# Kernel tuning notes

Hardware: AMD Instinct MI355X
Metric: run time of the kernel (lower is better)

Reference implementation:

```python
import jax, jax.numpy as jnp
import numpy as np

DIM = 512
HEADS = 16
HEAD_DIM = DIM // HEADS
WH, WW = 7, 7
N = WH * WW
OUP = 512
SCALE = HEAD_DIM ** -0.5
NW = 64  # windows per image (mask leading dim)


def _relative_position_index():
    coords = np.stack(np.meshgrid(np.arange(WH), np.arange(WW), indexing='ij'))  # (2,Wh,Ww)
    flat = coords.reshape(2, -1)                           # (2, N)
    rel = flat[:, :, None] - flat[:, None, :]              # (2, N, N)
    rel = rel.transpose(1, 2, 0).astype(np.int64)          # (N, N, 2)
    rel[:, :, 0] += WH - 1
    rel[:, :, 1] += WW - 1
    rel[:, :, 0] *= 2 * WW - 1
    return jnp.asarray(rel.sum(-1))                        # (N, N) int

REL_IDX = _relative_position_index()


def setup_inputs() -> dict:
    key = jax.random.key(0)
    ks = jax.random.split(key, 8)
    B_ = 4096
    x = jax.random.normal(ks[0], (B_, N, DIM), dtype=jnp.float32)
    mask = jnp.zeros((NW, N, N), dtype=jnp.float32)
    qkv_w = jax.random.normal(ks[1], (3 * DIM, DIM), dtype=jnp.float32) * (DIM ** -0.5)
    qkv_b = jax.random.normal(ks[2], (3 * DIM,), dtype=jnp.float32) * 0.02
    table = jax.random.normal(ks[3], ((2 * WH - 1) * (2 * WW - 1), HEADS), dtype=jnp.float32) * 0.02
    proj_w = jax.random.normal(ks[4], (OUP, DIM), dtype=jnp.float32) * (DIM ** -0.5)
    proj_b = jax.random.normal(ks[5], (OUP,), dtype=jnp.float32) * 0.02
    return {"x": x, "mask": mask, "qkv_w": qkv_w, "qkv_b": qkv_b,
            "table": table, "proj_w": proj_w, "proj_b": proj_b}


def reference(x, mask, qkv_w, qkv_b, table, proj_w, proj_b):
    B_, n, c = x.shape
    qkv = x @ qkv_w.T + qkv_b                               # (B_, N, 3C)
    qkv = qkv.reshape(B_, n, 3, HEADS, HEAD_DIM).transpose(2, 0, 3, 1, 4)
    q, k, v = qkv[0], qkv[1], qkv[2]                        # (B_, H, N, hd)
    q = q * SCALE
    attn = jnp.einsum('bhnd,bhmd->bhnm', q, k)              # (B_, H, N, N)
    bias = table[REL_IDX]                                   # (N, N, H) gather
    attn = attn + bias.transpose(2, 0, 1)[None]             # add rel-pos bias
    nW = mask.shape[0]
    attn = attn.reshape(B_ // nW, nW, HEADS, n, n) + mask[None, :, None]
    attn = attn.reshape(B_, HEADS, n, n)
    attn = jax.nn.softmax(attn, axis=-1)
    out = jnp.einsum('bhnm,bhmd->bhnd', attn, v)            # (B_, H, N, hd)
    out = out.transpose(0, 2, 1, 3).reshape(B_, n, c)
    return out @ proj_w.T + proj_b
```

## Files before the change

kernel.cpp:

```cpp
#include <hip/hip_runtime.h>
#include <hip/hip_bf16.h>
#include <stdint.h>

#define DIMC 512
#define HEADS 16
#define HEAD_DIM 32
#define NTOK 49
#define SCALE 0.17677669529663687f

typedef unsigned short u16;
typedef short bf16x8 __attribute__((ext_vector_type(8)));
typedef float f32x4 __attribute__((ext_vector_type(4)));
typedef u16 u16x4 __attribute__((ext_vector_type(4)));

#define MFMA16(a, b, c) __builtin_amdgcn_mfma_f32_16x16x32_bf16((a), (b), (c), 0, 0, 0)

__device__ __forceinline__ u16 f2bf(float f) {
  __hip_bfloat16 h = __float2bfloat16(f);
  u16 u;
  __builtin_memcpy(&u, &h, 2);
  return u;
}

__device__ __forceinline__ void gld16(const void* g, void* l) {
  __builtin_amdgcn_global_load_lds(
      (const __attribute__((address_space(1))) uint32_t*)g,
      (__attribute__((address_space(3))) uint32_t*)l, 16, 0, 0);
}

__global__ void cvt_f32_bf16(const float* __restrict__ in, u16* __restrict__ out, int n) {
  int i = (blockIdx.x * 256 + threadIdx.x) * 4;
  if (i < n) {
    float4 v = *(const float4*)(in + i);
    u16x4 r;
    r.x = f2bf(v.x); r.y = f2bf(v.y); r.z = f2bf(v.z); r.w = f2bf(v.w);
    *(u16x4*)(out + i) = r;
  }
}

__global__ void biasmask_kernel(const float* __restrict__ table, const float* __restrict__ mask,
                                float* __restrict__ bm) {
  const int wm = blockIdx.x >> 4;
  const int h  = blockIdx.x & 15;
  for (int e = threadIdx.x; e < 4096; e += 256) {
    const int i = e >> 6, j = e & 63;
    float v;
    if (i < NTOK && j < NTOK) {
      const int yi = i / 7, xi = i % 7, yj = j / 7, xj = j % 7;
      const int idx = (yi - yj + 6) * 13 + (xi - xj + 6);
      v = table[idx * HEADS + h] + mask[wm * (NTOK * NTOK) + i * NTOK + j];
    } else {
      v = -1e30f;
    }
    bm[(size_t)blockIdx.x * 4096 + e] = v;
  }
}

template<bool A_F32, bool OUT_BF16, bool QKV_SCALE>
__global__ void gemm_tn(const void* __restrict__ Ap, const u16* __restrict__ Bp,
                        const float* __restrict__ bias, void* __restrict__ Cp,
                        int M, int N, int K) {
  constexpr int ASTR = A_F32 ? 40 : 32;
  __shared__ u16 As[128 * ASTR];
  __shared__ u16 Bs[128 * 32];
  const int t = threadIdx.x;
  const int lane = t & 63;
  const int wv = t >> 6, wr = wv >> 1, wc = wv & 1;
  const int lr = lane & 15, lg = lane >> 4;
  const int bn0 = blockIdx.x * 128;
  const int bm0 = blockIdx.y * 128;

  f32x4 acc[4][4] = {};

  const int c0 = t, c1 = t + 256;
  const int nK = K >> 5;

  for (int kt = 0; kt < nK; ++kt) {
    const int k0 = kt << 5;
    __syncthreads();
    gld16(Bp + (size_t)(bn0 + (c0 >> 2)) * K + k0 + (c0 & 3) * 8, Bs + c0 * 8);
    gld16(Bp + (size_t)(bn0 + (c1 >> 2)) * K + k0 + (c1 & 3) * 8, Bs + c1 * 8);
    if (A_F32) {
      const float* A = (const float*)Ap;
      const float* src = A + (size_t)(bm0 + (t >> 1)) * K + k0 + (t & 1) * 16;
      float4 v0 = ((const float4*)src)[0];
      float4 v1 = ((const float4*)src)[1];
      float4 v2 = ((const float4*)src)[2];
      float4 v3 = ((const float4*)src)[3];
      bf16x8 p0, p1;
      p0[0] = f2bf(v0.x); p0[1] = f2bf(v0.y); p0[2] = f2bf(v0.z); p0[3] = f2bf(v0.w);
      p0[4] = f2bf(v1.x); p0[5] = f2bf(v1.y); p0[6] = f2bf(v1.z); p0[7] = f2bf(v1.w);
      p1[0] = f2bf(v2.x); p1[1] = f2bf(v2.y); p1[2] = f2bf(v2.z); p1[3] = f2bf(v2.w);
      p1[4] = f2bf(v3.x); p1[5] = f2bf(v3.y); p1[6] = f2bf(v3.z); p1[7] = f2bf(v3.w);
      u16* dst = &As[(t >> 1) * ASTR + (t & 1) * 16];
      *(bf16x8*)dst = p0;
      *(bf16x8*)(dst + 8) = p1;
    } else {
      const u16* A = (const u16*)Ap;
      gld16(A + (size_t)(bm0 + (c0 >> 2)) * K + k0 + (c0 & 3) * 8, As + c0 * 8);
      gld16(A + (size_t)(bm0 + (c1 >> 2)) * K + k0 + (c1 & 3) * 8, As + c1 * 8);
    }
    __syncthreads();

    bf16x8 af[4], bfr[4];
#pragma unroll
    for (int i = 0; i < 4; ++i)
      af[i] = *(const bf16x8*)&As[(wr * 64 + i * 16 + lr) * ASTR + lg * 8];
#pragma unroll
    for (int j = 0; j < 4; ++j)
      bfr[j] = *(const bf16x8*)&Bs[(wc * 64 + j * 16 + lr) * 32 + lg * 8];
#pragma unroll
    for (int i = 0; i < 4; ++i)
#pragma unroll
      for (int j = 0; j < 4; ++j)
        acc[i][j] = MFMA16(af[i], bfr[j], acc[i][j]);
  }

#pragma unroll
  for (int j = 0; j < 4; ++j) {
    const int col = bn0 + wc * 64 + j * 16 + lr;
    const float bv = bias[col];
    const float sc = (QKV_SCALE && col < DIMC) ? SCALE : 1.0f;
#pragma unroll
    for (int i = 0; i < 4; ++i) {
      const int row0 = bm0 + wr * 64 + i * 16 + lg * 4;
#pragma unroll
      for (int r = 0; r < 4; ++r) {
        const float val = (acc[i][j][r] + bv) * sc;
        if (OUT_BF16)
          ((u16*)Cp)[(size_t)(row0 + r) * N + col] = f2bf(val);
        else
          ((float*)Cp)[(size_t)(row0 + r) * N + col] = val;
      }
    }
  }
}

__global__ void attn_win(const u16* __restrict__ qkv, const float* __restrict__ bmask,
                         u16* __restrict__ aout) {
  __shared__ u16 P[4][64 * 72];
  const int t = threadIdx.x, lane = t & 63, wv = t >> 6;
  const int lr = lane & 15, lg = lane >> 4;
  const int w = blockIdx.x >> 2;
  const int h = ((blockIdx.x & 3) << 2) + wv;
  const size_t base = (size_t)w * NTOK * 1536 + h * HEAD_DIM;

  const bf16x8 zf = {};
  bf16x8 qf[4], kf[4];
#pragma unroll
  for (int i = 0; i < 4; ++i) {
    const int row = i * 16 + lr;
    const size_t roff = base + (size_t)row * 1536 + lg * 8;
    qf[i] = (row < NTOK) ? *(const bf16x8*)&qkv[roff] : zf;
    kf[i] = (row < NTOK) ? *(const bf16x8*)&qkv[roff + DIMC] : zf;
  }

  const f32x4 zc = {};
  f32x4 s[4][4];
#pragma unroll
  for (int i = 0; i < 4; ++i)
#pragma unroll
    for (int j = 0; j < 4; ++j)
      s[i][j] = MFMA16(qf[i], kf[j], zc);

  const float* bmp = bmask + (((size_t)(w & 63) * HEADS + h) << 12);
#pragma unroll
  for (int i = 0; i < 4; ++i)
#pragma unroll
    for (int r = 0; r < 4; ++r) {
      const int ii = i * 16 + lg * 4 + r;
#pragma unroll
      for (int j = 0; j < 4; ++j)
        s[i][j][r] += bmp[ii * 64 + j * 16 + lr];
    }

#pragma unroll
  for (int i = 0; i < 4; ++i)
#pragma unroll
    for (int r = 0; r < 4; ++r) {
      float m = fmaxf(fmaxf(s[i][0][r], s[i][1][r]), fmaxf(s[i][2][r], s[i][3][r]));
      m = fmaxf(m, __shfl_xor(m, 1));
      m = fmaxf(m, __shfl_xor(m, 2));
      m = fmaxf(m, __shfl_xor(m, 4));
      m = fmaxf(m, __shfl_xor(m, 8));
      float sum = 0.f;
#pragma unroll
      for (int j = 0; j < 4; ++j) {
        const float e = __expf(s[i][j][r] - m);
        s[i][j][r] = e;
        sum += e;
      }
      sum += __shfl_xor(sum, 1);
      sum += __shfl_xor(sum, 2);
      sum += __shfl_xor(sum, 4);
      sum += __shfl_xor(sum, 8);
      const float rinv = __builtin_amdgcn_rcpf(sum);
#pragma unroll
      for (int j = 0; j < 4; ++j) s[i][j][r] *= rinv;
    }

  u16* Pw = &P[wv][0];
#pragma unroll
  for (int i = 0; i < 4; ++i)
#pragma unroll
    for (int r = 0; r < 4; ++r) {
      const int ii = i * 16 + lg * 4 + r;
#pragma unroll
      for (int j = 0; j < 4; ++j)
        Pw[ii * 72 + j * 16 + lr] = f2bf(s[i][j][r]);
    }

  f32x4 o[4][2] = {};
#pragma unroll
  for (int ks = 0; ks < 2; ++ks) {
    bf16x8 vf[2];
#pragma unroll
    for (int dn = 0; dn < 2; ++dn) {
#pragma unroll
      for (int e = 0; e < 8; ++e) {
        int kk = ks * 32 + lg * 8 + e;
        kk = kk < NTOK ? kk : 0;
        vf[dn][e] = (short)qkv[base + 2 * DIMC + (size_t)kk * 1536 + dn * 16 + lr];
      }
    }
#pragma unroll
    for (int i = 0; i < 4; ++i) {
      const bf16x8 pa = *(const bf16x8*)&Pw[(i * 16 + lr) * 72 + ks * 32 + lg * 8];
#pragma unroll
      for (int dn = 0; dn < 2; ++dn)
        o[i][dn] = MFMA16(pa, vf[dn], o[i][dn]);
    }
  }

#pragma unroll
  for (int i = 0; i < 4; ++i)
#pragma unroll
    for (int r = 0; r < 4; ++r) {
      const int row = i * 16 + lg * 4 + r;
      if (row < NTOK) {
        const size_t ob = ((size_t)w * NTOK + row) * DIMC + h * HEAD_DIM;
#pragma unroll
        for (int dn = 0; dn < 2; ++dn)
          aout[ob + dn * 16 + lr] = f2bf(o[i][dn][r]);
      }
    }
}

extern "C" void kernel_launch(void* const* d_in, const int* in_sizes, int n_in,
                              void* d_out, int out_size, void* d_ws, size_t ws_size,
                              hipStream_t stream) {
  const float* x      = (const float*)d_in[0];
  const float* mask   = (const float*)d_in[1];
  const float* qkv_w  = (const float*)d_in[2];
  const float* qkv_b  = (const float*)d_in[3];
  const float* table  = (const float*)d_in[4];
  const float* proj_w = (const float*)d_in[5];
  const float* proj_b = (const float*)d_in[6];
  float* out = (float*)d_out;

  const int M = 4096 * NTOK;

  char* ws = (char*)d_ws;
  u16*   qkv_bf   = (u16*)ws;
  u16*   wqkv_bf  = (u16*)(ws + 616562688ull);
  u16*   wproj_bf = (u16*)(ws + 618135552ull);
  float* biasmask = (float*)(ws + 618659840ull);
  u16*   attn_bf  = (u16*)(ws + 635437056ull);

  cvt_f32_bf16<<<768, 256, 0, stream>>>(qkv_w, wqkv_bf, 1536 * 512);
  cvt_f32_bf16<<<256, 256, 0, stream>>>(proj_w, wproj_bf, 512 * 512);
  biasmask_kernel<<<1024, 256, 0, stream>>>(table, mask, biasmask);

  dim3 g1(1536 / 128, M / 128);
  gemm_tn<true, true, true><<<g1, 256, 0, stream>>>(x, wqkv_bf, qkv_b, qkv_bf, M, 1536, 512);

  attn_win<<<4096 * 4, 256, 0, stream>>>(qkv_bf, biasmask, attn_bf);

  dim3 g2(512 / 128, M / 128);
  gemm_tn<false, false, false><<<g2, 256, 0, stream>>>(attn_bf, wproj_bf, proj_b, out, M, 512, 512);
}
```

Before: 1.186 ms.

## Pre-convert x to bf16 and use swizzled K=64 GEMM tiles with block remapping

Adds a separate pass that converts x to bf16, so both GEMMs load their A operand through direct global-to-LDS loads instead of converting fp32 inside the tile loop. The GEMM now uses a 64-wide K tile with an XOR-swizzled LDS layout to avoid bank conflicts, and halves the number of barrier iterations. Blocks are launched on a 1D grid and remapped in strided groups of eight to improve L2 locality. The conversion kernel becomes a grid-stride loop handling eight elements per thread. The cost is an extra full read and write of x through the new conversion pass.

```diff
diff --git a/kernel.cpp b/kernel.cpp
--- a/kernel.cpp
+++ b/kernel.cpp
@@ -12,6 +12,7 @@
 typedef short bf16x8 __attribute__((ext_vector_type(8)));
 typedef float f32x4 __attribute__((ext_vector_type(4)));
 typedef u16 u16x4 __attribute__((ext_vector_type(4)));
+typedef u16 u16x8 __attribute__((ext_vector_type(8)));
 
 #define MFMA16(a, b, c) __builtin_amdgcn_mfma_f32_16x16x32_bf16((a), (b), (c), 0, 0, 0)
 
@@ -29,12 +30,14 @@
 }
 
 __global__ void cvt_f32_bf16(const float* __restrict__ in, u16* __restrict__ out, int n) {
-  int i = (blockIdx.x * 256 + threadIdx.x) * 4;
-  if (i < n) {
-    float4 v = *(const float4*)(in + i);
-    u16x4 r;
-    r.x = f2bf(v.x); r.y = f2bf(v.y); r.z = f2bf(v.z); r.w = f2bf(v.w);
-    *(u16x4*)(out + i) = r;
+  const int stride = gridDim.x * blockDim.x;
+  for (int i = blockIdx.x * blockDim.x + threadIdx.x; i * 8 < n; i += stride) {
+    const float4 v0 = ((const float4*)(in + i * 8))[0];
+    const float4 v1 = ((const float4*)(in + i * 8))[1];
+    u16x8 r;
+    r[0] = f2bf(v0.x); r[1] = f2bf(v0.y); r[2] = f2bf(v0.z); r[3] = f2bf(v0.w);
+    r[4] = f2bf(v1.x); r[5] = f2bf(v1.y); r[6] = f2bf(v1.z); r[7] = f2bf(v1.w);
+    *(u16x8*)(out + i * 8) = r;
   }
 }
 
@@ -56,64 +59,64 @@
   }
 }
 
-template<bool A_F32, bool OUT_BF16, bool QKV_SCALE>
-__global__ void gemm_tn(const void* __restrict__ Ap, const u16* __restrict__ Bp,
-                        const float* __restrict__ bias, void* __restrict__ Cp,
-                        int M, int N, int K) {
-  constexpr int ASTR = A_F32 ? 40 : 32;
-  __shared__ u16 As[128 * ASTR];
-  __shared__ u16 Bs[128 * 32];
+template<bool OUT_BF16, bool QKV_SCALE>
+__global__ void gemm_bf16(const u16* __restrict__ Ap, const u16* __restrict__ Bp,
+                          const float* __restrict__ bias, void* __restrict__ Cp,
+                          int M, int N, int K, int nxt) {
+  __shared__ u16 As[128 * 64];
+  __shared__ u16 Bs[128 * 64];
   const int t = threadIdx.x;
   const int lane = t & 63;
+  const int q = gridDim.x >> 3;
+  const int lin = blockIdx.x;
+  const int l = (lin & 7) * q + (lin >> 3);
+  const int bm0 = (l / nxt) * 128;
+  const int bn0 = (l % nxt) * 128;
   const int wv = t >> 6, wr = wv >> 1, wc = wv & 1;
   const int lr = lane & 15, lg = lane >> 4;
-  const int bn0 = blockIdx.x * 128;
-  const int bm0 = blockIdx.y * 128;
 
   f32x4 acc[4][4] = {};
 
-  const int c0 = t, c1 = t + 256;
-  const int nK = K >> 5;
-
+  int soff[4];
+#pragma unroll
+  for (int k = 0; k < 4; ++k) {
+    const int c = t + 256 * k;
+    const int row = c >> 3, sub = c & 7;
+    soff[k] = ((sub ^ (row & 7)) * 8);
+  }
+
+  const int nK = K >> 6;
   for (int kt = 0; kt < nK; ++kt) {
-    const int k0 = kt << 5;
+    const int k0 = kt << 6;
     __syncthreads();
-    gld16(Bp + (size_t)(bn0 + (c0 >> 2)) * K + k0 + (c0 & 3) * 8, Bs + c0 * 8);
-    gld16(Bp + (size_t)(bn0 + (c1 >> 2)) * K + k0 + (c1 & 3) * 8, Bs + c1 * 8);
-    if (A_F32) {
-      const float* A = (const float*)Ap;
-      const float* src = A + (size_t)(bm0 + (t >> 1)) * K + k0 + (t & 1) * 16;
-      float4 v0 = ((const float4*)src)[0];
-      float4 v1 = ((const float4*)src)[1];
-      float4 v2 = ((const float4*)src)[2];
-      float4 v3 = ((const float4*)src)[3];
-      bf16x8 p0, p1;
-      p0[0] = f2bf(v0.x); p0[1] = f2bf(v0.y); p0[2] = f2bf(v0.z); p0[3] = f2bf(v0.w);
-      p0[4] = f2bf(v1.x); p0[5] = f2bf(v1.y); p0[6] = f2bf(v1.z); p0[7] = f2bf(v1.w);
-      p1[0] = f2bf(v2.x); p1[1] = f2bf(v2.y); p1[2] = f2bf(v2.z); p1[3] = f2bf(v2.w);
-      p1[4] = f2bf(v3.x); p1[5] = f2bf(v3.y); p1[6] = f2bf(v3.z); p1[7] = f2bf(v3.w);
-      u16* dst = &As[(t >> 1) * ASTR + (t & 1) * 16];
-      *(bf16x8*)dst = p0;
-      *(bf16x8*)(dst + 8) = p1;
-    } else {
-      const u16* A = (const u16*)Ap;
-      gld16(A + (size_t)(bm0 + (c0 >> 2)) * K + k0 + (c0 & 3) * 8, As + c0 * 8);
-      gld16(A + (size_t)(bm0 + (c1 >> 2)) * K + k0 + (c1 & 3) * 8, As + c1 * 8);
+#pragma unroll
+    for (int k = 0; k < 4; ++k) {
+      const int c = t + 256 * k;
+      const int row = c >> 3;
+      gld16(Ap + (size_t)(bm0 + row) * K + k0 + soff[k], As + c * 8);
+      gld16(Bp + (size_t)(bn0 + row) * K + k0 + soff[k], Bs + c * 8);
     }
     __syncthreads();
 
-    bf16x8 af[4], bfr[4];
-#pragma unroll
-    for (int i = 0; i < 4; ++i)
-      af[i] = *(const bf16x8*)&As[(wr * 64 + i * 16 + lr) * ASTR + lg * 8];
-#pragma unroll
-    for (int j = 0; j < 4; ++j)
-      bfr[j] = *(const bf16x8*)&Bs[(wc * 64 + j * 16 + lr) * 32 + lg * 8];
-#pragma unroll
-    for (int i = 0; i < 4; ++i)
-#pragma unroll
-      for (int j = 0; j < 4; ++j)
-        acc[i][j] = MFMA16(af[i], bfr[j], acc[i][j]);
+#pragma unroll
+    for (int kk = 0; kk < 2; ++kk) {
+      bf16x8 af[4], bfr[4];
+#pragma unroll
+      for (int i = 0; i < 4; ++i) {
+        const int row = wr * 64 + i * 16 + lr;
+        af[i] = *(const bf16x8*)&As[row * 64 + ((kk * 4 + lg) ^ (row & 7)) * 8];
+      }
+#pragma unroll
+      for (int j = 0; j < 4; ++j) {
+        const int row = wc * 64 + j * 16 + lr;
+        bfr[j] = *(const bf16x8*)&Bs[row * 64 + ((kk * 4 + lg) ^ (row & 7)) * 8];
+      }
+#pragma unroll
+      for (int i = 0; i < 4; ++i)
+#pragma unroll
+        for (int j = 0; j < 4; ++j)
+          acc[i][j] = MFMA16(af[i], bfr[j], acc[i][j]);
+    }
   }
 
 #pragma unroll
@@ -265,17 +268,19 @@
   u16*   wqkv_bf  = (u16*)(ws + 616562688ull);
   u16*   wproj_bf = (u16*)(ws + 618135552ull);
   float* biasmask = (float*)(ws + 618659840ull);
-  u16*   attn_bf  = (u16*)(ws + 635437056ull);
+  u16*   x_bf     = (u16*)(ws + 635437056ull);
+  u16*   attn_bf  = x_bf;
 
   cvt_f32_bf16<<<768, 256, 0, stream>>>(qkv_w, wqkv_bf, 1536 * 512);
   cvt_f32_bf16<<<256, 256, 0, stream>>>(proj_w, wproj_bf, 512 * 512);
   biasmask_kernel<<<1024, 256, 0, stream>>>(table, mask, biasmask);
-
-  dim3 g1(1536 / 128, M / 128);
-  gemm_tn<true, true, true><<<g1, 256, 0, stream>>>(x, wqkv_bf, qkv_b, qkv_bf, M, 1536, 512);
+  cvt_f32_bf16<<<1792, 256, 0, stream>>>(x, x_bf, M * DIMC);
+
+  gemm_bf16<true, true><<<1568 * 12, 256, 0, stream>>>(
+      x_bf, wqkv_bf, qkv_b, qkv_bf, M, 1536, 512, 12);
 
   attn_win<<<4096 * 4, 256, 0, stream>>>(qkv_bf, biasmask, attn_bf);
 
-  dim3 g2(512 / 128, M / 128);
-  gemm_tn<false, false, false><<<g2, 256, 0, stream>>>(attn_bf, wproj_bf, proj_b, out, M, 512, 512);
-}
+  gemm_bf16<false, false><<<1568 * 4, 256, 0, stream>>>(
+      attn_bf, wproj_bf, proj_b, out, M, 512, 512, 4);
+}
```

New measurement: 1.012 ms. 14.6% less time.
